# Performance work log

Hardware: AMD Instinct MI355X
Metric: run time of the kernel (lower is better)

The kernel has to match this reference:

```python
import jax, jax.numpy as jnp
import numpy as np

NB_OBJ = 3
DIM_BODY = 10
DIM_OBJ = 15
DIM_LEMB = 100
PHI_IN = DIM_LEMB + DIM_BODY + 2 * (NB_OBJ + DIM_OBJ)  # 146
HID = 256
PHI_OUT = 256
ACT_DIM = 4
BATCH = 65536
LOG_SIG_MIN, LOG_SIG_MAX = -20.0, 2.0
# permutations of 3 objects taken 2: (0,1),(0,2),(1,0),(1,2),(2,0),(2,1)
IDX_I = np.array([0, 0, 1, 1, 2, 2])
IDX_J = np.array([1, 2, 0, 2, 0, 1])


def _xavier(key, fan_in, fan_out):
    lim = float(np.sqrt(6.0 / (fan_in + fan_out)))
    return jax.random.uniform(key, (fan_in, fan_out), jnp.float32, -lim, lim)


def setup_inputs() -> dict:
    key = jax.random.key(0)
    ks = jax.random.split(key, 8)
    return {
        "obs": jax.random.normal(ks[0], (BATCH, DIM_BODY + NB_OBJ * DIM_OBJ), jnp.float32),
        "l_emb": jax.random.normal(ks[1], (BATCH, DIM_LEMB), jnp.float32),
        "phi_w1": _xavier(ks[2], PHI_IN, HID), "phi_b1": jnp.zeros((HID,), jnp.float32),
        "phi_w2": _xavier(ks[3], HID, PHI_OUT), "phi_b2": jnp.zeros((PHI_OUT,), jnp.float32),
        "rho_w1": _xavier(ks[4], PHI_OUT, HID), "rho_b1": jnp.zeros((HID,), jnp.float32),
        "mean_w": _xavier(ks[5], HID, ACT_DIM), "mean_b": jnp.zeros((ACT_DIM,), jnp.float32),
        "lstd_w": _xavier(ks[6], HID, ACT_DIM), "lstd_b": jnp.zeros((ACT_DIM,), jnp.float32),
    }


def reference(obs, l_emb, phi_w1, phi_b1, phi_w2, phi_b2,
              rho_w1, rho_b1, mean_w, mean_b, lstd_w, lstd_b):
    B = obs.shape[0]
    obs_body = obs[:, :DIM_BODY]                                   # [B, 10]
    obj_feats = obs[:, DIM_BODY:].reshape(B, NB_OBJ, DIM_OBJ)      # [B, 3, 15]
    one_hot = jnp.broadcast_to(jnp.eye(NB_OBJ, dtype=obs.dtype)[None], (B, NB_OBJ, NB_OBJ))
    objs = jnp.concatenate([one_hot, obj_feats], axis=-1)          # [B, 3, 18]
    base = jnp.concatenate([l_emb, obs_body], axis=-1)             # [B, 110]
    # pairwise concat over the 6 ordered pairs -> [6, B, 146]
    xi = objs[:, IDX_I].transpose(1, 0, 2)                         # [6, B, 18]
    xj = objs[:, IDX_J].transpose(1, 0, 2)
    base6 = jnp.broadcast_to(base[None], (6, B, base.shape[-1]))
    inp = jnp.concatenate([base6, xi, xj], axis=-1)                # [6, B, 146]
    # phi MLP
    h = jax.nn.relu(jnp.einsum('pbi,ih->pbh', inp, phi_w1) + phi_b1)
    h = jax.nn.relu(jnp.einsum('pbh,ho->pbo', h, phi_w2) + phi_b2)
    agg = h.sum(axis=0)                                            # [B, 256]
    # rho MLP
    r = jax.nn.relu(agg @ rho_w1 + rho_b1)
    mean = r @ mean_w + mean_b
    log_std = jnp.clip(r @ lstd_w + lstd_b, LOG_SIG_MIN, LOG_SIG_MAX)
    return mean, log_std
```

## Files before the change

kernel.cpp:

```cpp
#include <hip/hip_runtime.h>

#define BATCH 65536
#define TB 32

typedef _Float16 half8 __attribute__((ext_vector_type(8)));
typedef _Float16 half4v __attribute__((ext_vector_type(4)));
typedef _Float16 half2v __attribute__((ext_vector_type(2)));
typedef float fx4 __attribute__((ext_vector_type(4)));

#define PW1B_OFF 0
#define PW1F_OFF 32768
#define PW2_OFF  40960
#define PWR_OFF  106496
#define PWH_OFF  172032
#define WS_TOTAL 176128

__global__ __launch_bounds__(256) void prep_weights(
    const float* __restrict__ w1, const float* __restrict__ w2,
    const float* __restrict__ wr, const float* __restrict__ wm,
    const float* __restrict__ wl, _Float16* __restrict__ ws)
{
  int idx = blockIdx.x * 256 + threadIdx.x;
  if (idx < 32768) {
    int kk = idx & 31, n = (idx >> 5) & 255, kt = idx >> 13;
    int k = kt * 32 + kk;
    ws[idx] = (k < 110) ? (_Float16)w1[k * 256 + n] : (_Float16)0.f;
  } else if (idx < 40960) {
    int t = idx - 32768;
    int kk = t & 31, n = t >> 5;
    _Float16 v = (_Float16)0.f;
    if (kk < 15)                  v = (_Float16)w1[(113 + kk) * 256 + n];
    else if (kk >= 16 && kk < 31) v = (_Float16)w1[(131 + (kk - 16)) * 256 + n];
    ws[idx] = v;
  } else if (idx < 106496) {
    int t = idx - 40960;
    int kk = t & 31, n = (t >> 5) & 255, kt = t >> 13;
    ws[idx] = (_Float16)w2[(kt * 32 + kk) * 256 + n];
  } else if (idx < 172032) {
    int t = idx - 106496;
    int kk = t & 31, n = (t >> 5) & 255, kt = t >> 13;
    ws[idx] = (_Float16)wr[(kt * 32 + kk) * 256 + n];
  } else if (idx < WS_TOTAL) {
    int t = idx - 172032;
    int kk = t & 31, n = (t >> 5) & 15, kt = t >> 9;
    int k = kt * 32 + kk;
    _Float16 v = (_Float16)0.f;
    if (n < 4) v = (_Float16)wm[k * 4 + n];
    else if (n < 8) v = (_Float16)wl[k * 4 + (n - 4)];
    ws[PWH_OFF + t] = v;
  }
}

__global__ __launch_bounds__(512) __attribute__((amdgpu_waves_per_eu(4, 4)))
void actor_fused(
    const float* __restrict__ obs, const float* __restrict__ lemb,
    const float* __restrict__ w1, const _Float16* __restrict__ ws,
    const float* __restrict__ b1, const float* __restrict__ b2,
    const float* __restrict__ br, const float* __restrict__ bm,
    const float* __restrict__ bl, float* __restrict__ out)
{
  __shared__ __align__(16) _Float16 H1[6 * 16 * 256];
  __shared__ __align__(16) _Float16 Bb[32 * 256];
  __shared__ __align__(16) _Float16 Os[3 * 32 * 16];
  __shared__ __align__(16) float    Bsf[6 * 256];

  const _Float16* __restrict__ pw1b = ws + PW1B_OFF;
  const _Float16* __restrict__ pw1f = ws + PW1F_OFF;
  const _Float16* __restrict__ pw2  = ws + PW2_OFF;
  const _Float16* __restrict__ pwr  = ws + PWR_OFF;
  const _Float16* __restrict__ pwh  = ws + PWH_OFF;

  const int tid  = threadIdx.x;
  const int wave = tid >> 6;
  const int lane = tid & 63;
  const int q    = lane >> 4;
  const int l16  = lane & 15;
  const int colbase = wave * 32;
  const int rowbase = blockIdx.x * TB;

  const int c0_0 = colbase + q * 4;
  const int c0_1 = colbase + 16 + q * 4;

  for (int idx = tid; idx < 1024; idx += 512) {
    int oct = idx >> 6;
    int r   = (idx >> 1) & 31;
    int hf  = idx & 1;
    int c   = oct * 8 + hf * 4;
    float v0, v1, v2, v3;
    if (c + 3 < 100) {
      float4 f = *(const float4*)(lemb + (rowbase + r) * 100 + c);
      v0 = f.x; v1 = f.y; v2 = f.z; v3 = f.w;
    } else {
      const float* orow = obs + (rowbase + r) * 55;
      const float* lrow = lemb + (rowbase + r) * 100;
      float t[4];
      #pragma unroll
      for (int j = 0; j < 4; ++j) {
        int cc = c + j;
        t[j] = cc < 100 ? lrow[cc] : (cc < 110 ? orow[cc - 100] : 0.f);
      }
      v0 = t[0]; v1 = t[1]; v2 = t[2]; v3 = t[3];
    }
    half4v hv = {(_Float16)v0, (_Float16)v1, (_Float16)v2, (_Float16)v3};
    *(half4v*)&Bb[(oct * 32 + r) * 8 + hf * 4] = hv;
  }
  for (int idx = tid; idx < 384; idx += 512) {
    int o   = idx >> 7;
    int k4i = (idx >> 5) & 3;
    int r   = idx & 31;
    int k0  = k4i * 4;
    const float* frow = obs + (rowbase + r) * 55 + 10 + o * 15;
    float t[4];
    #pragma unroll
    for (int j = 0; j < 4; ++j) {
      int k = k0 + j;
      t[j] = (k < 15) ? frow[k] : 0.f;
    }
    half4v hv = {(_Float16)t[0], (_Float16)t[1], (_Float16)t[2], (_Float16)t[3]};
    *(half4v*)&Os[o * 512 + ((k0 >> 3) * 32 + r) * 8 + (k0 & 7)] = hv;
  }
  for (int idx = tid; idx < 1536; idx += 512) {
    int p = idx >> 8, c = idx & 255;
    int oi = p >> 1, oj = (1161 >> (2 * p)) & 3;
    Bsf[idx] = b1[c] + w1[(110 + oi) * 256 + c] + w1[(128 + oj) * 256 + c];
  }
  __syncthreads();

  const fx4 zero4 = {0.f, 0.f, 0.f, 0.f};

  fx4 u[4];
  u[0] = zero4; u[1] = zero4; u[2] = zero4; u[3] = zero4;
  #pragma unroll
  for (int kt = 0; kt < 4; ++kt) {
    half8 a0 = *(const half8*)&Bb[((kt * 4 + q) * 32 + l16) * 8];
    half8 a1 = *(const half8*)&Bb[((kt * 4 + q) * 32 + 16 + l16) * 8];
    #pragma unroll
    for (int nt = 0; nt < 2; ++nt) {
      half8 b = *(const half8*)&pw1b[(kt * 256 + colbase + nt * 16 + l16) * 32 + q * 8];
      u[nt]     = __builtin_amdgcn_mfma_f32_16x16x32_f16(b, a0, u[nt], 0, 0, 0);
      u[2 + nt] = __builtin_amdgcn_mfma_f32_16x16x32_f16(b, a1, u[2 + nt], 0, 0, 0);
    }
  }

  auto g1_group = [&](int g) {
    half8 b1f0 = *(const half8*)&pw1f[(colbase + l16) * 32 + q * 8];
    half8 b1f1 = *(const half8*)&pw1f[(colbase + 16 + l16) * 32 + q * 8];
    #pragma unroll
    for (int pp = 0; pp < 3; ++pp) {
      const int p = g * 3 + pp;
      const int oi = p >> 1, oj = (1161 >> (2 * p)) & 3;
      const int o = (q < 2) ? oi : oj;
      #pragma unroll
      for (int rt = 0; rt < 2; ++rt) {
        half8 af = *(const half8*)&Os[o * 512 + ((q & 1) * 32 + rt * 16 + l16) * 8];
        #pragma unroll
        for (int nt = 0; nt < 2; ++nt) {
          fx4 t = __builtin_amdgcn_mfma_f32_16x16x32_f16(nt ? b1f1 : b1f0, af,
                                                         u[rt * 2 + nt], 0, 0, 0);
          const int c0 = nt ? c0_1 : c0_0;
          fx4 bs = *(const fx4*)&Bsf[p * 256 + c0];
          half4v hv = {(_Float16)fmaxf(t[0] + bs[0], 0.f),
                       (_Float16)fmaxf(t[1] + bs[1], 0.f),
                       (_Float16)fmaxf(t[2] + bs[2], 0.f),
                       (_Float16)fmaxf(t[3] + bs[3], 0.f)};
          *(half4v*)&H1[(pp * 2 + rt) * 4096 + ((c0 >> 3) * 16 + l16) * 8 + (c0 & 7)] = hv;
        }
      }
    }
  };

  fx4 agg[4];
  agg[0] = zero4; agg[1] = zero4; agg[2] = zero4; agg[3] = zero4;

  auto g2_group = [&]() {
    const _Float16* wp0 = &pw2[(colbase + l16) * 32 + q * 8];
    const _Float16* wp1 = wp0 + 16 * 32;
    fx4 bv0 = *(const fx4*)&b2[c0_0];
    fx4 bv1 = *(const fx4*)&b2[c0_1];
    fx4 acc[12];
    #pragma unroll
    for (int i = 0; i < 12; ++i) acc[i] = (i & 1) ? bv1 : bv0;
    #pragma unroll
    for (int kt = 0; kt < 8; ++kt) {
      half8 a[6];
      #pragma unroll
      for (int t6 = 0; t6 < 6; ++t6)
        a[t6] = *(const half8*)&H1[t6 * 4096 + ((kt * 4 + q) * 16 + l16) * 8];
      half8 bb0 = *(const half8*)(wp0 + kt * 8192);
      half8 bb1 = *(const half8*)(wp1 + kt * 8192);
      #pragma unroll
      for (int t6 = 0; t6 < 6; ++t6) {
        acc[t6 * 2]     = __builtin_amdgcn_mfma_f32_16x16x32_f16(bb0, a[t6], acc[t6 * 2], 0, 0, 0);
        acc[t6 * 2 + 1] = __builtin_amdgcn_mfma_f32_16x16x32_f16(bb1, a[t6], acc[t6 * 2 + 1], 0, 0, 0);
      }
    }
    #pragma unroll
    for (int t6 = 0; t6 < 6; ++t6)
      #pragma unroll
      for (int nt = 0; nt < 2; ++nt)
        #pragma unroll
        for (int rr = 0; rr < 4; ++rr)
          agg[(t6 & 1) * 2 + nt][rr] += fmaxf(acc[t6 * 2 + nt][rr], 0.f);
  };

  g1_group(0);
  __syncthreads();
  g2_group();
  __syncthreads();
  g1_group(1);
  __syncthreads();
  g2_group();

  #pragma unroll
  for (int rt = 0; rt < 2; ++rt)
    #pragma unroll
    for (int nt = 0; nt < 2; ++nt) {
      const int c0 = nt ? c0_1 : c0_0;
      fx4 t = agg[rt * 2 + nt];
      half4v hv = {(_Float16)t[0], (_Float16)t[1], (_Float16)t[2], (_Float16)t[3]};
      *(half4v*)&Bb[((c0 >> 3) * 32 + rt * 16 + l16) * 8 + (c0 & 7)] = hv;
    }
  __syncthreads();

  fx4 acc3[4];
  {
    fx4 brv0 = *(const fx4*)&br[c0_0];
    fx4 brv1 = *(const fx4*)&br[c0_1];
    acc3[0] = brv0; acc3[1] = brv1; acc3[2] = brv0; acc3[3] = brv1;
  }
  #pragma unroll
  for (int kt = 0; kt < 8; ++kt) {
    half8 a0 = *(const half8*)&Bb[((kt * 4 + q) * 32 + l16) * 8];
    half8 a1 = *(const half8*)&Bb[((kt * 4 + q) * 32 + 16 + l16) * 8];
    half8 b0 = *(const half8*)&pwr[(kt * 256 + colbase + l16) * 32 + q * 8];
    half8 b1h = *(const half8*)&pwr[(kt * 256 + colbase + 16 + l16) * 32 + q * 8];
    acc3[0] = __builtin_amdgcn_mfma_f32_16x16x32_f16(b0,  a0, acc3[0], 0, 0, 0);
    acc3[1] = __builtin_amdgcn_mfma_f32_16x16x32_f16(b1h, a0, acc3[1], 0, 0, 0);
    acc3[2] = __builtin_amdgcn_mfma_f32_16x16x32_f16(b0,  a1, acc3[2], 0, 0, 0);
    acc3[3] = __builtin_amdgcn_mfma_f32_16x16x32_f16(b1h, a1, acc3[3], 0, 0, 0);
  }
  #pragma unroll
  for (int rt = 0; rt < 2; ++rt)
    #pragma unroll
    for (int nt = 0; nt < 2; ++nt) {
      const int c0 = nt ? c0_1 : c0_0;
      fx4 t = acc3[rt * 2 + nt];
      half4v hv = {(_Float16)fmaxf(t[0], 0.f), (_Float16)fmaxf(t[1], 0.f),
                   (_Float16)fmaxf(t[2], 0.f), (_Float16)fmaxf(t[3], 0.f)};
      *(half4v*)&H1[rt * 4096 + ((c0 >> 3) * 16 + l16) * 8 + (c0 & 7)] = hv;
    }
  __syncthreads();

  if (wave < 2) {
    fx4 a4 = zero4;
    #pragma unroll
    for (int kt = 0; kt < 8; ++kt) {
      half8 rfrag = *(const half8*)&H1[wave * 4096 + ((kt * 4 + q) * 16 + l16) * 8];
      half8 wfrag = *(const half8*)&pwh[(kt * 16 + l16) * 32 + q * 8];
      a4 = __builtin_amdgcn_mfma_f32_16x16x32_f16(wfrag, rfrag, a4, 0, 0, 0);
    }
    const int row = rowbase + wave * 16 + l16;
    if (q == 0) {
      fx4 bm4 = *(const fx4*)bm;
      fx4 o = {a4[0] + bm4[0], a4[1] + bm4[1], a4[2] + bm4[2], a4[3] + bm4[3]};
      *(fx4*)&out[row * 4] = o;
    } else if (q == 1) {
      fx4 bl4 = *(const fx4*)bl;
      fx4 o;
      #pragma unroll
      for (int rr = 0; rr < 4; ++rr) {
        float v = a4[rr] + bl4[rr];
        o[rr] = v < -20.f ? -20.f : (v > 2.f ? 2.f : v);
      }
      *(fx4*)&out[BATCH * 4 + row * 4] = o;
    }
  }
}

extern "C" void kernel_launch(void* const* d_in, const int* in_sizes, int n_in,
                              void* d_out, int out_size, void* d_ws, size_t ws_size,
                              hipStream_t stream) {
  const float* obs  = (const float*)d_in[0];
  const float* lemb = (const float*)d_in[1];
  const float* w1   = (const float*)d_in[2];
  const float* b1   = (const float*)d_in[3];
  const float* w2   = (const float*)d_in[4];
  const float* b2   = (const float*)d_in[5];
  const float* wr   = (const float*)d_in[6];
  const float* br   = (const float*)d_in[7];
  const float* wm   = (const float*)d_in[8];
  const float* bm   = (const float*)d_in[9];
  const float* wl   = (const float*)d_in[10];
  const float* bl   = (const float*)d_in[11];
  float* out = (float*)d_out;
  _Float16* ws = (_Float16*)d_ws;

  hipLaunchKernelGGL(prep_weights, dim3(WS_TOTAL / 256), dim3(256), 0, stream,
                     w1, w2, wr, wm, wl, ws);
  hipLaunchKernelGGL(actor_fused, dim3(BATCH / TB), dim3(512), 0, stream,
                     obs, lemb, w1, (const _Float16*)ws, b1, b2, br, bm, bl, out);
}
```

Baseline: 204.9 us.

## Process pairs in groups of two with recomputed base term to cut registers and LDS

Restructures the phi stage to handle the six object pairs in three groups of two instead of two groups of three. H1 shrinks from 6 to 4 tiles and the layer-2 accumulators from 12 to 8. The shared base GEMM term is recomputed per group instead of held live, the running aggregate is kept in fp16 registers, and several loops are only partially unrolled. It also drops the fixed waves-per-EU attribute. The aim is lower register and LDS pressure, paid for with redundant base-GEMM work, an extra barrier round, and fp16 rounding of the partial sums.

```diff
diff --git a/kernel.cpp b/kernel.cpp
--- a/kernel.cpp
+++ b/kernel.cpp
@@ -51,15 +51,14 @@
   }
 }
 
-__global__ __launch_bounds__(512) __attribute__((amdgpu_waves_per_eu(4, 4)))
-void actor_fused(
+__global__ __launch_bounds__(512) void actor_fused(
     const float* __restrict__ obs, const float* __restrict__ lemb,
     const float* __restrict__ w1, const _Float16* __restrict__ ws,
     const float* __restrict__ b1, const float* __restrict__ b2,
     const float* __restrict__ br, const float* __restrict__ bm,
     const float* __restrict__ bl, float* __restrict__ out)
 {
-  __shared__ __align__(16) _Float16 H1[6 * 16 * 256];
+  __shared__ __align__(16) _Float16 H1[4 * 16 * 256];
   __shared__ __align__(16) _Float16 Bb[32 * 256];
   __shared__ __align__(16) _Float16 Os[3 * 32 * 16];
   __shared__ __align__(16) float    Bsf[6 * 256];
@@ -128,26 +127,27 @@
 
   const fx4 zero4 = {0.f, 0.f, 0.f, 0.f};
 
-  fx4 u[4];
-  u[0] = zero4; u[1] = zero4; u[2] = zero4; u[3] = zero4;
-  #pragma unroll
-  for (int kt = 0; kt < 4; ++kt) {
-    half8 a0 = *(const half8*)&Bb[((kt * 4 + q) * 32 + l16) * 8];
-    half8 a1 = *(const half8*)&Bb[((kt * 4 + q) * 32 + 16 + l16) * 8];
-    #pragma unroll
-    for (int nt = 0; nt < 2; ++nt) {
-      half8 b = *(const half8*)&pw1b[(kt * 256 + colbase + nt * 16 + l16) * 32 + q * 8];
-      u[nt]     = __builtin_amdgcn_mfma_f32_16x16x32_f16(b, a0, u[nt], 0, 0, 0);
-      u[2 + nt] = __builtin_amdgcn_mfma_f32_16x16x32_f16(b, a1, u[2 + nt], 0, 0, 0);
-    }
-  }
-
-  auto g1_group = [&](int g) {
+  auto compute_u = [&](fx4* u) {
+    u[0] = zero4; u[1] = zero4; u[2] = zero4; u[3] = zero4;
+    #pragma unroll
+    for (int kt = 0; kt < 4; ++kt) {
+      half8 a0 = *(const half8*)&Bb[((kt * 4 + q) * 32 + l16) * 8];
+      half8 a1 = *(const half8*)&Bb[((kt * 4 + q) * 32 + 16 + l16) * 8];
+      #pragma unroll
+      for (int nt = 0; nt < 2; ++nt) {
+        half8 b = *(const half8*)&pw1b[(kt * 256 + colbase + nt * 16 + l16) * 32 + q * 8];
+        u[nt]     = __builtin_amdgcn_mfma_f32_16x16x32_f16(b, a0, u[nt], 0, 0, 0);
+        u[2 + nt] = __builtin_amdgcn_mfma_f32_16x16x32_f16(b, a1, u[2 + nt], 0, 0, 0);
+      }
+    }
+  };
+
+  auto g1_pair = [&](int g, const fx4* u) {
     half8 b1f0 = *(const half8*)&pw1f[(colbase + l16) * 32 + q * 8];
     half8 b1f1 = *(const half8*)&pw1f[(colbase + 16 + l16) * 32 + q * 8];
     #pragma unroll
-    for (int pp = 0; pp < 3; ++pp) {
-      const int p = g * 3 + pp;
+    for (int pp = 0; pp < 2; ++pp) {
+      const int p = g * 2 + pp;
       const int oi = p >> 1, oj = (1161 >> (2 * p)) & 3;
       const int o = (q < 2) ? oi : oj;
       #pragma unroll
@@ -169,56 +169,71 @@
     }
   };
 
-  fx4 agg[4];
-  agg[0] = zero4; agg[1] = zero4; agg[2] = zero4; agg[3] = zero4;
-
-  auto g2_group = [&]() {
-    const _Float16* wp0 = &pw2[(colbase + l16) * 32 + q * 8];
-    const _Float16* wp1 = wp0 + 16 * 32;
+  half4v aggp[4];
+  {
+    half4v z = {(_Float16)0.f, (_Float16)0.f, (_Float16)0.f, (_Float16)0.f};
+    aggp[0] = z; aggp[1] = z; aggp[2] = z; aggp[3] = z;
+  }
+
+  auto g2_pair = [&]() {
     fx4 bv0 = *(const fx4*)&b2[c0_0];
     fx4 bv1 = *(const fx4*)&b2[c0_1];
-    fx4 acc[12];
-    #pragma unroll
-    for (int i = 0; i < 12; ++i) acc[i] = (i & 1) ? bv1 : bv0;
-    #pragma unroll
+    fx4 acc[8];
+    #pragma unroll
+    for (int i = 0; i < 8; ++i) acc[i] = (i & 1) ? bv1 : bv0;
+    #pragma unroll 2
     for (int kt = 0; kt < 8; ++kt) {
-      half8 a[6];
-      #pragma unroll
-      for (int t6 = 0; t6 < 6; ++t6)
-        a[t6] = *(const half8*)&H1[t6 * 4096 + ((kt * 4 + q) * 16 + l16) * 8];
-      half8 bb0 = *(const half8*)(wp0 + kt * 8192);
-      half8 bb1 = *(const half8*)(wp1 + kt * 8192);
-      #pragma unroll
-      for (int t6 = 0; t6 < 6; ++t6) {
-        acc[t6 * 2]     = __builtin_amdgcn_mfma_f32_16x16x32_f16(bb0, a[t6], acc[t6 * 2], 0, 0, 0);
-        acc[t6 * 2 + 1] = __builtin_amdgcn_mfma_f32_16x16x32_f16(bb1, a[t6], acc[t6 * 2 + 1], 0, 0, 0);
-      }
-    }
-    #pragma unroll
-    for (int t6 = 0; t6 < 6; ++t6)
-      #pragma unroll
-      for (int nt = 0; nt < 2; ++nt)
+      half8 bb0 = *(const half8*)&pw2[(kt * 256 + colbase + l16) * 32 + q * 8];
+      half8 bb1 = *(const half8*)&pw2[(kt * 256 + colbase + 16 + l16) * 32 + q * 8];
+      #pragma unroll
+      for (int t4 = 0; t4 < 4; ++t4) {
+        half8 a = *(const half8*)&H1[t4 * 4096 + ((kt * 4 + q) * 16 + l16) * 8];
+        acc[t4 * 2]     = __builtin_amdgcn_mfma_f32_16x16x32_f16(bb0, a, acc[t4 * 2], 0, 0, 0);
+        acc[t4 * 2 + 1] = __builtin_amdgcn_mfma_f32_16x16x32_f16(bb1, a, acc[t4 * 2 + 1], 0, 0, 0);
+      }
+    }
+    #pragma unroll
+    for (int rt = 0; rt < 2; ++rt)
+      #pragma unroll
+      for (int nt = 0; nt < 2; ++nt) {
+        int i = rt * 2 + nt;
+        fx4 s;
         #pragma unroll
-        for (int rr = 0; rr < 4; ++rr)
-          agg[(t6 & 1) * 2 + nt][rr] += fmaxf(acc[t6 * 2 + nt][rr], 0.f);
+        for (int rr = 0; rr < 4; ++rr) s[rr] = (float)aggp[i][rr];
+        #pragma unroll
+        for (int rr = 0; rr < 4; ++rr) {
+          s[rr] += fmaxf(acc[rt * 2 + nt][rr], 0.f);
+          s[rr] += fmaxf(acc[(2 + rt) * 2 + nt][rr], 0.f);
+        }
+        half4v hv = {(_Float16)s[0], (_Float16)s[1], (_Float16)s[2], (_Float16)s[3]};
+        aggp[i] = hv;
+      }
   };
 
-  g1_group(0);
-  __syncthreads();
-  g2_group();
-  __syncthreads();
-  g1_group(1);
-  __syncthreads();
-  g2_group();
+  {
+    fx4 u[4];
+    compute_u(u);
+    g1_pair(0, u);
+    __syncthreads();
+    g2_pair();
+    compute_u(u);
+    __syncthreads();
+    g1_pair(1, u);
+    __syncthreads();
+    g2_pair();
+    compute_u(u);
+    __syncthreads();
+    g1_pair(2, u);
+    __syncthreads();
+    g2_pair();
+  }
 
   #pragma unroll
   for (int rt = 0; rt < 2; ++rt)
     #pragma unroll
     for (int nt = 0; nt < 2; ++nt) {
       const int c0 = nt ? c0_1 : c0_0;
-      fx4 t = agg[rt * 2 + nt];
-      half4v hv = {(_Float16)t[0], (_Float16)t[1], (_Float16)t[2], (_Float16)t[3]};
-      *(half4v*)&Bb[((c0 >> 3) * 32 + rt * 16 + l16) * 8 + (c0 & 7)] = hv;
+      *(half4v*)&Bb[((c0 >> 3) * 32 + rt * 16 + l16) * 8 + (c0 & 7)] = aggp[rt * 2 + nt];
     }
   __syncthreads();
 
@@ -228,7 +243,7 @@
     fx4 brv1 = *(const fx4*)&br[c0_1];
     acc3[0] = brv0; acc3[1] = brv1; acc3[2] = brv0; acc3[3] = brv1;
   }
-  #pragma unroll
+  #pragma unroll 2
   for (int kt = 0; kt < 8; ++kt) {
     half8 a0 = *(const half8*)&Bb[((kt * 4 + q) * 32 + l16) * 8];
     half8 a1 = *(const half8*)&Bb[((kt * 4 + q) * 32 + 16 + l16) * 8];
@@ -253,7 +268,7 @@
 
   if (wave < 2) {
     fx4 a4 = zero4;
-    #pragma unroll
+    #pragma unroll 2
     for (int kt = 0; kt < 8; ++kt) {
       half8 rfrag = *(const half8*)&H1[wave * 4096 + ((kt * 4 + q) * 16 + l16) * 8];
       half8 wfrag = *(const half8*)&pwh[(kt * 16 + l16) * 32 + q * 8];
```

New measurement: 219.3 us. 1.07x slower.
